# Performance work log

Measured on AMD Instinct MI355X. Metric: run time of the kernel, lower is better.

## Reference

```python
import jax, jax.numpy as jnp
import numpy as np

N = 50000        # n_nodes
E = 1_600_000    # n_edges (before self-loops)
D_IN, HID, HEADS, D_OUT = 32, 64, 4, 32
NEG_SLOPE = 0.2  # PyG GATConv default leaky_relu slope


def setup_inputs() -> dict:
    key = jax.random.key(0)
    ks = jax.random.split(key, 10)
    x = jax.random.normal(ks[0], (N, D_IN), jnp.float32)
    edge_index = jax.random.randint(ks[1], (2, E), 0, N, dtype=jnp.int64)
    s = 0.1
    W_gcn = jax.random.normal(ks[2], (D_IN, HID), jnp.float32) * s
    b_gcn = jnp.zeros((HID,), jnp.float32)
    W_gat = jax.random.normal(ks[3], (HID, HEADS * HID), jnp.float32) * s
    att_src = jax.random.normal(ks[4], (HEADS, HID), jnp.float32) * s
    att_dst = jax.random.normal(ks[5], (HEADS, HID), jnp.float32) * s
    b_gat = jnp.zeros((HEADS * HID,), jnp.float32)
    W_fc = jax.random.normal(ks[6], (HEADS * HID, D_OUT), jnp.float32) * s
    b_fc = jnp.zeros((D_OUT,), jnp.float32)
    return dict(x=x, edge_index=edge_index, W_gcn=W_gcn, b_gcn=b_gcn,
                W_gat=W_gat, att_src=att_src, att_dst=att_dst, b_gat=b_gat,
                W_fc=W_fc, b_fc=b_fc)


def _add_self_loops(edge_index, n):
    loop = jnp.arange(n, dtype=edge_index.dtype)
    src = jnp.concatenate([edge_index[0], loop])
    dst = jnp.concatenate([edge_index[1], loop])
    return src, dst


def _gcn(x, src, dst, W, b):
    h = x @ W                                               # (N, HID)
    deg = jax.ops.segment_sum(jnp.ones_like(src, jnp.float32), dst, N)
    dinv = jnp.where(deg > 0, jax.lax.rsqrt(deg), 0.0)
    norm = dinv[src] * dinv[dst]                            # (E+N,)
    out = jax.ops.segment_sum(h[src] * norm[:, None], dst, N)
    return out + b


def _gat(x, src, dst, W, att_src, att_dst, b):
    h = (x @ W).reshape(N, HEADS, HID)                      # (N, H, C)
    a_s = jnp.einsum('nhc,hc->nh', h, att_src)              # (N, H)
    a_d = jnp.einsum('nhc,hc->nh', h, att_dst)
    e = jax.nn.leaky_relu(a_s[src] + a_d[dst], NEG_SLOPE)   # (E+N, H)
    # softmax over incoming edges per destination node
    m = jax.ops.segment_max(e, dst, N)                      # every dst has a self-loop
    w = jnp.exp(e - m[dst])
    denom = jax.ops.segment_sum(w, dst, N)
    alpha = w / denom[dst]                                  # (E+N, H)
    out = jax.ops.segment_sum(h[src] * alpha[:, :, None], dst, N)
    return out.reshape(N, HEADS * HID) + b


def reference(x, edge_index, W_gcn, b_gcn, W_gat, att_src, att_dst, b_gat, W_fc, b_fc):
    src, dst = _add_self_loops(edge_index, N)
    h = jax.nn.relu(_gcn(x, src, dst, W_gcn, b_gcn))        # dropout: eval mode (identity)
    h = jax.nn.relu(_gat(h, src, dst, W_gat, att_src, att_dst, b_gat))
    return h @ W_fc + b_fc
```

## Files before the change

### kernel.cpp

```cpp
#include <hip/hip_runtime.h>
#include <hip/hip_bf16.h>
#include <hip/hip_fp16.h>
#include <math.h>

#define N_NODES 50000
#define N_EDGES 1600000
#define D_IN    32
#define HID     64
#define HEADS   4
#define D_OUT   32
#define NEG_SLOPE 0.2f
#define CHUNK 128
#define NTILES 3125

#define NBKT 196
#define NBLK_A 391
#define TILE_A 4096
#define GH (NBKT * NBLK_A)
#define NSB 300
#define CAP 10240

typedef _Float16 half8 __attribute__((ext_vector_type(8)));
typedef float    f32x4 __attribute__((ext_vector_type(4)));
typedef float    f32x2 __attribute__((ext_vector_type(2)));

__global__ __launch_bounds__(256) void histA(const int* __restrict__ edge,
                                             int* __restrict__ ghist) {
    __shared__ int hist[4][NBKT];
    int t = threadIdx.x, wv = t >> 6;
    for (int i = t; i < 4 * NBKT; i += 256) ((int*)hist)[i] = 0;
    __syncthreads();
    int base = blockIdx.x * TILE_A;
#pragma unroll
    for (int k = 0; k < 16; k++) {
        int i = base + k * 256 + t;
        if (i < N_EDGES) atomicAdd(&hist[wv][edge[N_EDGES + i] >> 8], 1);
    }
    __syncthreads();
    for (int b = t; b < NBKT; b += 256)
        ghist[b * NBLK_A + blockIdx.x] = hist[0][b] + hist[1][b] + hist[2][b] + hist[3][b];
}

__global__ __launch_bounds__(256) void scanB1(const int* __restrict__ g,
                                              int* __restrict__ bsum) {
    int t = threadIdx.x;
    int i = blockIdx.x * 256 + t;
    int v = (i < GH) ? g[i] : 0;
#pragma unroll
    for (int off = 32; off; off >>= 1) v += __shfl_xor(v, off);
    __shared__ int ws[4];
    if ((t & 63) == 0) ws[t >> 6] = v;
    __syncthreads();
    if (t == 0) bsum[blockIdx.x] = ws[0] + ws[1] + ws[2] + ws[3];
}

__global__ __launch_bounds__(320) void scanB2_attvec(int* __restrict__ bsum,
                                                     const float* __restrict__ W,
                                                     const float* __restrict__ att_s,
                                                     const float* __restrict__ att_d,
                                                     float* __restrict__ vsrc,
                                                     float* __restrict__ vdst) {
    int t = threadIdx.x, lane = t & 63, wv = t >> 6;
    if (blockIdx.x == 0) {
        int v = (t < NSB) ? bsum[t] : 0;
        int inc = v;
#pragma unroll
        for (int d = 1; d < 64; d <<= 1) {
            int u = __shfl_up(inc, d);
            if (lane >= d) inc += u;
        }
        __shared__ int ws[5];
        if (lane == 63) ws[wv] = inc;
        __syncthreads();
        int add = 0;
#pragma unroll
        for (int j = 0; j < 5; j++) if (j < wv) add += ws[j];
        if (t < NSB) bsum[t] = add + inc - v;
    } else if (t < 256) {
        int h = t >> 6, k = t & 63;
        float s_ = 0.f, d_ = 0.f;
#pragma unroll 8
        for (int c = 0; c < 64; c++) {
            float w = W[k * 256 + h * 64 + c];
            s_ += w * att_s[h * 64 + c];
            d_ += w * att_d[h * 64 + c];
        }
        vsrc[h * 64 + k] = s_;
        vdst[h * 64 + k] = d_;
    }
}

__global__ __launch_bounds__(256) void scanB3(int* __restrict__ g,
                                              const int* __restrict__ bsum) {
    int t = threadIdx.x, lane = t & 63, wv = t >> 6;
    int i = blockIdx.x * 256 + t;
    int v = (i < GH) ? g[i] : 0;
    int inc = v;
#pragma unroll
    for (int d = 1; d < 64; d <<= 1) {
        int u = __shfl_up(inc, d);
        if (lane >= d) inc += u;
    }
    __shared__ int ws[4];
    if (lane == 63) ws[wv] = inc;
    __syncthreads();
    int add = 0;
#pragma unroll
    for (int j = 0; j < 4; j++) if (j < wv) add += ws[j];
    if (i < GH) g[i] = bsum[blockIdx.x] + add + inc - v;
}

__global__ __launch_bounds__(256) void scatterC(const int* __restrict__ edge,
                                                const int* __restrict__ ghist,
                                                unsigned* __restrict__ tmp) {
    __shared__ int cur[NBKT];
    int t = threadIdx.x;
    if (t < NBKT) cur[t] = ghist[t * NBLK_A + blockIdx.x];
    __syncthreads();
    int base = blockIdx.x * TILE_A;
#pragma unroll
    for (int k = 0; k < 16; k++) {
        int i = base + k * 256 + t;
        if (i < N_EDGES) {
            int s = edge[i], d = edge[N_EDGES + i];
            int pos = atomicAdd(&cur[d >> 8], 1);
            tmp[pos] = ((unsigned)d << 16) | (unsigned)s;
        }
    }
}

__global__ __launch_bounds__(256) void sortD(const unsigned* __restrict__ tmp,
                                             const int* __restrict__ ghist,
                                             unsigned short* __restrict__ colidx,
                                             int* __restrict__ rowptr,
                                             float* __restrict__ dinv) {
    __shared__ unsigned char  dl8[CAP];
    __shared__ unsigned short s16[CAP];
    __shared__ unsigned short o16[CAP];
    __shared__ int hist[4][256];
    __shared__ int excl[256];
    __shared__ int wsum[4];
    int t = threadIdx.x, lane = t & 63, wv = t >> 6;
    int b = blockIdx.x;
    int lo = ghist[b * NBLK_A];
    int hi = (b < NBKT - 1) ? ghist[(b + 1) * NBLK_A] : N_EDGES;
    int size = hi - lo;
    if (size > CAP) size = CAP;
    for (int i = t; i < 4 * 256; i += 256) ((int*)hist)[i] = 0;
    __syncthreads();
    for (int i = t; i < size; i += 256) {
        unsigned key = tmp[lo + i];
        int dl = (key >> 16) & 255;
        dl8[i] = (unsigned char)dl;
        s16[i] = (unsigned short)(key & 0xFFFF);
        atomicAdd(&hist[wv][dl], 1);
    }
    __syncthreads();
    int h = hist[0][t] + hist[1][t] + hist[2][t] + hist[3][t];
    int inc = h;
#pragma unroll
    for (int d = 1; d < 64; d <<= 1) {
        int u = __shfl_up(inc, d);
        if (lane >= d) inc += u;
    }
    if (lane == 63) wsum[wv] = inc;
    __syncthreads();
    int add = 0;
#pragma unroll
    for (int j = 0; j < 4; j++) if (j < wv) add += wsum[j];
    int ex = inc - h + add;
    excl[t] = ex;
    int node = b * 256 + t;
    if (node < N_NODES) {
        rowptr[node] = lo + ex;
        dinv[node]   = rsqrtf((float)(h + 1));
    }
    if (b == NBKT - 1 && t == 0) rowptr[N_NODES] = N_EDGES;
    __syncthreads();
    for (int i = t; i < size; i += 256) {
        int pos = atomicAdd(&excl[dl8[i]], 1);
        o16[pos] = s16[i];
    }
    __syncthreads();
    for (int i = t; i < size; i += 256) colidx[lo + i] = o16[i];
}

__global__ __launch_bounds__(256) void gemm1(const float* __restrict__ x,
                                             const float* __restrict__ W,
                                             const float* __restrict__ dinv,
                                             __half* __restrict__ h,
                                             __half* __restrict__ h1) {
    __shared__ float Wl[D_IN * HID];
    int t = threadIdx.x;
    if (blockIdx.x == 0 && t < HID) {
        h [(size_t)N_NODES * HID + t] = __float2half(0.f);
        h1[(size_t)N_NODES * HID + t] = __float2half(0.f);
    }
    for (int i = t; i < D_IN * HID; i += 256) Wl[i] = W[i];
    __syncthreads();
    int c = t & 63, rw = t >> 6;
    int r0 = blockIdx.x * 32;
#pragma unroll
    for (int rr = 0; rr < 8; rr++) {
        int r = r0 + rr * 4 + rw;
        if (r >= N_NODES) break;
        const float4* xr4 = (const float4*)(x + r * D_IN);
        float acc = 0.f;
#pragma unroll
        for (int k4 = 0; k4 < D_IN / 4; k4++) {
            float4 xv = xr4[k4];
            int k = k4 * 4;
            acc += xv.x * Wl[(k+0)*HID + c] + xv.y * Wl[(k+1)*HID + c]
                 + xv.z * Wl[(k+2)*HID + c] + xv.w * Wl[(k+3)*HID + c];
        }
        h[r * HID + c] = __float2half(acc * dinv[r]);
    }
}

__global__ __launch_bounds__(256) void gcn_agg(const __half* __restrict__ h,
                                               const int* __restrict__ rowptr,
                                               const unsigned short* __restrict__ colidx,
                                               const float* __restrict__ dinv,
                                               const float* __restrict__ b,
                                               const float* __restrict__ vsrc,
                                               const float* __restrict__ vdst,
                                               __half* __restrict__ h1,
                                               float* __restrict__ as_o,
                                               float* __restrict__ ad_o) {
    __shared__ int sbuf[4][CHUNK + 4];
    int lane = threadIdx.x & 63, wv = threadIdx.x >> 6;
    int quarter = lane >> 4, ql = lane & 15;
    int n = blockIdx.x * 4 + wv;
    if (n >= N_NODES) return;
    int rp = rowptr[n], re = rowptr[n + 1];
    f32x2 a01 = {0.f, 0.f}, a23 = {0.f, 0.f};
    const __half* hp = h + ql * 4;
    for (int cb = rp; cb < re; cb += CHUNK) {
        int ce = min(cb + CHUNK, re);
        for (int e = cb + lane; e < ce; e += 64) sbuf[wv][e - cb] = colidx[e];
        int m = ce - cb;
        int pad = (4 - (m & 3)) & 3;
        if (lane < pad) sbuf[wv][m + lane] = N_NODES;
        int m4 = (m + pad) >> 2;
#pragma unroll 2
        for (int i = 0; i < m4; i++) {
            int s = sbuf[wv][i * 4 + quarter];
            float2 raw = *(const float2*)(hp + s * HID);
            __half2 g0 = __builtin_bit_cast(__half2, raw.x);
            __half2 g1 = __builtin_bit_cast(__half2, raw.y);
            float2 f0 = __half22float2(g0), f1 = __half22float2(g1);
            a01.x += f0.x; a01.y += f0.y;
            a23.x += f1.x; a23.y += f1.y;
        }
    }
#pragma unroll
    for (int off = 16; off <= 32; off <<= 1) {
        a01.x += __shfl_xor(a01.x, off); a01.y += __shfl_xor(a01.y, off);
        a23.x += __shfl_xor(a23.x, off); a23.y += __shfl_xor(a23.y, off);
    }
    if (quarter == 0) {
        float2 raw = *(const float2*)(hp + n * HID);
        __half2 g0 = __builtin_bit_cast(__half2, raw.x);
        __half2 g1 = __builtin_bit_cast(__half2, raw.y);
        float2 f0 = __half22float2(g0), f1 = __half22float2(g1);
        a01.x += f0.x; a01.y += f0.y;
        a23.x += f1.x; a23.y += f1.y;
    }
    float dn = dinv[n];
    const float4 bb = *(const float4*)&b[ql * 4];
    float v0 = fmaxf(a01.x * dn + bb.x, 0.f);
    float v1 = fmaxf(a01.y * dn + bb.y, 0.f);
    float v2 = fmaxf(a23.x * dn + bb.z, 0.f);
    float v3 = fmaxf(a23.y * dn + bb.w, 0.f);
    if (quarter == 0) {
        __half2* op = (__half2*)&h1[n * HID + ql * 4];
        op[0] = __floats2half2_rn(v0, v1);
        op[1] = __floats2half2_rn(v2, v3);
    }
#pragma unroll
    for (int hh = 0; hh < 4; hh++) {
        float4 vsp = *(const float4*)&vsrc[hh * 64 + ql * 4];
        float4 vdp = *(const float4*)&vdst[hh * 64 + ql * 4];
        float vs = v0 * vsp.x + v1 * vsp.y + v2 * vsp.z + v3 * vsp.w;
        float vd = v0 * vdp.x + v1 * vdp.y + v2 * vdp.z + v3 * vdp.w;
#pragma unroll
        for (int off = 8; off > 0; off >>= 1) {
            vs += __shfl_xor(vs, off);
            vd += __shfl_xor(vd, off);
        }
        if (lane == 0) {
            as_o[n * 4 + hh] = vs;
            ad_o[n * 4 + hh] = vd;
        }
    }
}

__global__ __launch_bounds__(256) void gat_agg(const __half* __restrict__ h1,
                                               const int* __restrict__ rowptr,
                                               const unsigned short* __restrict__ colidx,
                                               const float* __restrict__ a_s,
                                               const float* __restrict__ a_d,
                                               __half* __restrict__ u) {
    __shared__ float wbuf[4][(CHUNK + 4) * 4];
    __shared__ int   sbuf[4][CHUNK + 4];
    int lane = threadIdx.x & 63, wv = threadIdx.x >> 6;
    int quarter = lane >> 4, ql = lane & 15;
    int n = blockIdx.x * 4 + wv;
    if (n >= N_NODES) return;
    int rp = rowptr[n], re = rowptr[n + 1];
    float4 ad4 = *(const float4*)&a_d[n * 4];
    float4 asn = *(const float4*)&a_s[n * 4];

    float dnx = 0.f, dny = 0.f, dnz = 0.f, dnw = 0.f;
    f32x2 acc[4][2];
#pragma unroll
    for (int hh = 0; hh < 4; hh++) { acc[hh][0] = (f32x2){0.f,0.f}; acc[hh][1] = (f32x2){0.f,0.f}; }
    const __half* hp = h1 + ql * 4;
    for (int cb = rp; cb < re; cb += CHUNK) {
        int ce = min(cb + CHUNK, re);
        for (int e = cb + lane; e < ce; e += 64) {
            int s = colidx[e];
            float4 a = *(const float4*)&a_s[s * 4];
            float vx = a.x + ad4.x; vx = fmaxf(vx, NEG_SLOPE * vx);
            float vy = a.y + ad4.y; vy = fmaxf(vy, NEG_SLOPE * vy);
            float vz = a.z + ad4.z; vz = fmaxf(vz, NEG_SLOPE * vz);
            float vw = a.w + ad4.w; vw = fmaxf(vw, NEG_SLOPE * vw);
            float wx = __expf(vx), wy = __expf(vy);
            float wz = __expf(vz), ww = __expf(vw);
            dnx += wx; dny += wy; dnz += wz; dnw += ww;
            int idx = e - cb;
            *(float4*)&wbuf[wv][idx * 4] = make_float4(wx, wy, wz, ww);
            sbuf[wv][idx] = s;
        }
        int m = ce - cb;
        int pad = (4 - (m & 3)) & 3;
        if (lane < pad) {
            sbuf[wv][m + lane] = N_NODES;
            *(float4*)&wbuf[wv][(m + lane) * 4] = make_float4(0.f, 0.f, 0.f, 0.f);
        }
        int m4 = (m + pad) >> 2;
#pragma unroll 2
        for (int i = 0; i < m4; i++) {
            int idx = i * 4 + quarter;
            int s = sbuf[wv][idx];
            float4 w4 = *(const float4*)&wbuf[wv][idx * 4];
            float2 raw = *(const float2*)(hp + s * HID);
            __half2 g0 = __builtin_bit_cast(__half2, raw.x);
            __half2 g1 = __builtin_bit_cast(__half2, raw.y);
            float2 t0 = __half22float2(g0), t1 = __half22float2(g1);
            f32x2 f0 = {t0.x, t0.y}, f1 = {t1.x, t1.y};
            f32x2 wx2 = {w4.x, w4.x}, wy2 = {w4.y, w4.y};
            f32x2 wz2 = {w4.z, w4.z}, ww2 = {w4.w, w4.w};
            acc[0][0] += wx2 * f0; acc[0][1] += wx2 * f1;
            acc[1][0] += wy2 * f0; acc[1][1] += wy2 * f1;
            acc[2][0] += wz2 * f0; acc[2][1] += wz2 * f1;
            acc[3][0] += ww2 * f0; acc[3][1] += ww2 * f1;
        }
    }
#pragma unroll
    for (int hh = 0; hh < 4; hh++)
#pragma unroll
        for (int c = 0; c < 2; c++) {
            acc[hh][c].x += __shfl_xor(acc[hh][c].x, 16);
            acc[hh][c].y += __shfl_xor(acc[hh][c].y, 16);
            acc[hh][c].x += __shfl_xor(acc[hh][c].x, 32);
            acc[hh][c].y += __shfl_xor(acc[hh][c].y, 32);
        }
#pragma unroll
    for (int off = 32; off > 0; off >>= 1) {
        dnx += __shfl_xor(dnx, off);
        dny += __shfl_xor(dny, off);
        dnz += __shfl_xor(dnz, off);
        dnw += __shfl_xor(dnw, off);
    }
    float sx = asn.x + ad4.x; sx = fmaxf(sx, NEG_SLOPE * sx);
    float sy = asn.y + ad4.y; sy = fmaxf(sy, NEG_SLOPE * sy);
    float sz = asn.z + ad4.z; sz = fmaxf(sz, NEG_SLOPE * sz);
    float sw = asn.w + ad4.w; sw = fmaxf(sw, NEG_SLOPE * sw);
    float wsx = __expf(sx), wsy = __expf(sy);
    float wsz = __expf(sz), wsw = __expf(sw);
    dnx += wsx; dny += wsy; dnz += wsz; dnw += wsw;
    if (quarter == 0) {
        float2 raw = *(const float2*)(hp + n * HID);
        __half2 g0 = __builtin_bit_cast(__half2, raw.x);
        __half2 g1 = __builtin_bit_cast(__half2, raw.y);
        float2 t0 = __half22float2(g0), t1 = __half22float2(g1);
        acc[0][0].x += wsx * t0.x; acc[0][0].y += wsx * t0.y; acc[0][1].x += wsx * t1.x; acc[0][1].y += wsx * t1.y;
        acc[1][0].x += wsy * t0.x; acc[1][0].y += wsy * t0.y; acc[1][1].x += wsy * t1.x; acc[1][1].y += wsy * t1.y;
        acc[2][0].x += wsz * t0.x; acc[2][0].y += wsz * t0.y; acc[2][1].x += wsz * t1.x; acc[2][1].y += wsz * t1.y;
        acc[3][0].x += wsw * t0.x; acc[3][0].y += wsw * t0.y; acc[3][1].x += wsw * t1.x; acc[3][1].y += wsw * t1.y;
        float r4[4] = {1.f / dnx, 1.f / dny, 1.f / dnz, 1.f / dnw};
        __half* up = u + n * 256 + ql * 4;
#pragma unroll
        for (int hh = 0; hh < 4; hh++) {
            __half2* op = (__half2*)&up[hh * 64];
            op[0] = __floats2half2_rn(acc[hh][0].x * r4[hh], acc[hh][0].y * r4[hh]);
            op[1] = __floats2half2_rn(acc[hh][1].x * r4[hh], acc[hh][1].y * r4[hh]);
        }
    }
}

__global__ __launch_bounds__(256) void gemm2b(const __half* __restrict__ u,
                                              const float* __restrict__ W,
                                              const float* __restrict__ b,
                                              __half* __restrict__ h2) {
    int lane = threadIdx.x & 63, hd = threadIdx.x >> 6;
    int quad = lane >> 4, l16 = lane & 15;
    half8 Bf[4][2];
#pragma unroll
    for (int nt = 0; nt < 4; nt++)
#pragma unroll
        for (int kc = 0; kc < 2; kc++) {
            const float* wp = W + (kc * 32 + quad * 8) * 256 + hd * 64 + nt * 16 + l16;
#pragma unroll
            for (int j = 0; j < 8; j++)
                Bf[nt][kc][j] = (_Float16)wp[j * 256];
        }
    float bb[4];
#pragma unroll
    for (int nt = 0; nt < 4; nt++) bb[nt] = b[hd * 64 + nt * 16 + l16];

    int rt0 = blockIdx.x * 5;
#pragma unroll
    for (int i = 0; i < 5; i++) {
        int rt = rt0 + i;
        const __half* up = u + ((size_t)(rt * 16 + l16)) * 256 + hd * 64 + quad * 8;
        half8 A0 = *(const half8*)(const void*)up;
        half8 A1 = *(const half8*)(const void*)(up + 32);
        f32x4 acc[4];
#pragma unroll
        for (int nt = 0; nt < 4; nt++) {
            acc[nt] = (f32x4){0.f, 0.f, 0.f, 0.f};
            acc[nt] = __builtin_amdgcn_mfma_f32_16x16x32_f16(A0, Bf[nt][0], acc[nt], 0, 0, 0);
            acc[nt] = __builtin_amdgcn_mfma_f32_16x16x32_f16(A1, Bf[nt][1], acc[nt], 0, 0, 0);
        }
#pragma unroll
        for (int nt = 0; nt < 4; nt++) {
            int col = hd * 64 + nt * 16 + l16;
#pragma unroll
            for (int reg = 0; reg < 4; reg++) {
                int row = rt * 16 + quad * 4 + reg;
                h2[(size_t)row * 256 + col] = __float2half(fmaxf(acc[nt][reg] + bb[nt], 0.f));
            }
        }
    }
}

__global__ __launch_bounds__(256) void gemm3(const __half* __restrict__ h2,
                                             const float* __restrict__ W,
                                             const float* __restrict__ b,
                                             float* __restrict__ out) {
    int lane = threadIdx.x & 63, wv = threadIdx.x >> 6;
    int quad = lane >> 4, l16 = lane & 15;
    half8 Bf[2][8];
#pragma unroll
    for (int nt = 0; nt < 2; nt++)
#pragma unroll
        for (int kc = 0; kc < 8; kc++) {
            const float* wp = W + (kc * 32 + quad * 8) * 32 + nt * 16 + l16;
#pragma unroll
            for (int j = 0; j < 8; j++)
                Bf[nt][kc][j] = (_Float16)wp[j * 32];
        }
    float bb0 = b[l16], bb1 = b[16 + l16];

    for (int tile = blockIdx.x * 4 + wv; tile < NTILES; tile += gridDim.x * 4) {
        const __half* hp = h2 + (size_t)(tile * 16 + l16) * 256 + quad * 8;
        f32x4 acc0 = {0.f, 0.f, 0.f, 0.f};
        f32x4 acc1 = {0.f, 0.f, 0.f, 0.f};
#pragma unroll
        for (int kc = 0; kc < 8; kc++) {
            half8 A = *(const half8*)(const void*)(hp + kc * 32);
            acc0 = __builtin_amdgcn_mfma_f32_16x16x32_f16(A, Bf[0][kc], acc0, 0, 0, 0);
            acc1 = __builtin_amdgcn_mfma_f32_16x16x32_f16(A, Bf[1][kc], acc1, 0, 0, 0);
        }
#pragma unroll
        for (int reg = 0; reg < 4; reg++) {
            int row = tile * 16 + quad * 4 + reg;
            out[row * 32 + l16]      = acc0[reg] + bb0;
            out[row * 32 + 16 + l16] = acc1[reg] + bb1;
        }
    }
}

extern "C" void kernel_launch(void* const* d_in, const int* in_sizes, int n_in,
                              void* d_out, int out_size, void* d_ws, size_t ws_size,
                              hipStream_t stream) {
    const float* x      = (const float*)d_in[0];
    const int*   edge   = (const int*)  d_in[1];
    const float* W_gcn  = (const float*)d_in[2];
    const float* b_gcn  = (const float*)d_in[3];
    const float* W_gat  = (const float*)d_in[4];
    const float* att_s  = (const float*)d_in[5];
    const float* att_d  = (const float*)d_in[6];
    const float* b_gat  = (const float*)d_in[7];
    const float* W_fc   = (const float*)d_in[8];
    const float* b_fc   = (const float*)d_in[9];
    float* out = (float*)d_out;

    char* p = (char*)d_ws;
    auto alloc = [&](size_t bytes) {
        char* q = p;
        p += (bytes + 255) & ~(size_t)255;
        return q;
    };
    __half* h     = (__half*)alloc((size_t)(N_NODES + 1) * HID * 2);
    __half* h1    = (__half*)alloc((size_t)(N_NODES + 1) * HID * 2);
    __half* u     = (__half*)alloc((size_t)N_NODES * 256 * 2);
    __half* h2    = (__half*)alloc((size_t)N_NODES * 256 * 2);
    float* as_a   = (float*)alloc((size_t)N_NODES * 4 * 4);
    float* ad_a   = (float*)alloc((size_t)N_NODES * 4 * 4);
    float* dinv   = (float*)alloc((size_t)N_NODES * 4);
    int*   rowptr = (int*)  alloc((size_t)(N_NODES + 1) * 4);
    unsigned short* colidx = (unsigned short*)alloc((size_t)N_EDGES * 2);
    int*   ghist  = (int*)  alloc((size_t)GH * 4);
    int*   bsum   = (int*)  alloc((size_t)NSB * 4);
    unsigned* tmp = (unsigned*)alloc((size_t)N_EDGES * 4);
    float* vsrc   = (float*)alloc((size_t)HEADS * HID * 4);
    float* vdst   = (float*)alloc((size_t)HEADS * HID * 4);

    histA        <<<NBLK_A, 256, 0, stream>>>(edge, ghist);
    scanB1       <<<NSB, 256, 0, stream>>>(ghist, bsum);
    scanB2_attvec<<<2, 320, 0, stream>>>(bsum, W_gat, att_s, att_d, vsrc, vdst);
    scanB3       <<<NSB, 256, 0, stream>>>(ghist, bsum);
    scatterC     <<<NBLK_A, 256, 0, stream>>>(edge, ghist, tmp);
    sortD        <<<NBKT, 256, 0, stream>>>(tmp, ghist, colidx, rowptr, dinv);

    gemm1   <<<(N_NODES + 31) / 32, 256, 0, stream>>>(x, W_gcn, dinv, h, h1);
    gcn_agg <<<(N_NODES + 3) / 4, 256, 0, stream>>>(h, rowptr, colidx, dinv, b_gcn,
                                                    vsrc, vdst, h1, as_a, ad_a);

    gat_agg <<<(N_NODES + 3) / 4, 256, 0, stream>>>(h1, rowptr, colidx, as_a, ad_a, u);
    gemm2b  <<<625, 256, 0, stream>>>(u, W_gat, b_gat, h2);

    gemm3   <<<256, 256, 0, stream>>>(h2, W_fc, b_fc, out);
}
```

Measured before the change: 252.3 us.

## Map one node per quarter-wave in GCN and GAT aggregation kernels

Both aggregation kernels now assign each 16-lane quarter of a wavefront its own destination node (16 nodes per block) instead of one node per wavefront. Each quarter stages its own neighbor indices (premultiplied by HID) and attention weights in shared memory and walks them serially, padding up to the wavefront's maximum degree. This removes the cross-quarter shuffle reductions and the quarter-0-only epilogue, keeping all lanes busy on output. In exchange, degree imbalance among the four nodes in a wavefront causes wasted padded iterations. The bounds check on n was removed, which is safe only because N is divisible by 16.

```diff
diff --git a/kernel.cpp b/kernel.cpp
--- a/kernel.cpp
+++ b/kernel.cpp
@@ -10,8 +10,9 @@
 #define HEADS   4
 #define D_OUT   32
 #define NEG_SLOPE 0.2f
-#define CHUNK 128
 #define NTILES 3125
+
+#define CQ 64
 
 #define NBKT 196
 #define NBLK_A 391
@@ -227,25 +228,29 @@
                                                __half* __restrict__ h1,
                                                float* __restrict__ as_o,
                                                float* __restrict__ ad_o) {
-    __shared__ int sbuf[4][CHUNK + 4];
+    __shared__ int sbuf[4][4][CQ + 1];
     int lane = threadIdx.x & 63, wv = threadIdx.x >> 6;
     int quarter = lane >> 4, ql = lane & 15;
-    int n = blockIdx.x * 4 + wv;
-    if (n >= N_NODES) return;
+    int n = blockIdx.x * 16 + wv * 4 + quarter;
     int rp = rowptr[n], re = rowptr[n + 1];
+    int deg = re - rp;
+    int dm = deg;
+    dm = max(dm, __shfl_xor(dm, 16));
+    dm = max(dm, __shfl_xor(dm, 32));
     f32x2 a01 = {0.f, 0.f}, a23 = {0.f, 0.f};
     const __half* hp = h + ql * 4;
-    for (int cb = rp; cb < re; cb += CHUNK) {
-        int ce = min(cb + CHUNK, re);
-        for (int e = cb + lane; e < ce; e += 64) sbuf[wv][e - cb] = colidx[e];
-        int m = ce - cb;
-        int pad = (4 - (m & 3)) & 3;
-        if (lane < pad) sbuf[wv][m + lane] = N_NODES;
-        int m4 = (m + pad) >> 2;
-#pragma unroll 2
-        for (int i = 0; i < m4; i++) {
-            int s = sbuf[wv][i * 4 + quarter];
-            float2 raw = *(const float2*)(hp + s * HID);
+    int* sq = sbuf[wv][quarter];
+    for (int cb = 0; cb < dm; cb += CQ) {
+        int m  = min(CQ, max(deg - cb, 0));
+        int mm = min(CQ, dm - cb);
+        for (int j = ql; j < m; j += 16)
+            sq[j] = (int)colidx[rp + cb + j] * HID;
+        for (int j = m + ql; j < mm; j += 16)
+            sq[j] = N_NODES * HID;
+#pragma unroll 4
+        for (int i = 0; i < mm; i++) {
+            int off = sq[i];
+            float2 raw = *(const float2*)(hp + off);
             __half2 g0 = __builtin_bit_cast(__half2, raw.x);
             __half2 g1 = __builtin_bit_cast(__half2, raw.y);
             float2 f0 = __half22float2(g0), f1 = __half22float2(g1);
@@ -253,12 +258,7 @@
             a23.x += f1.x; a23.y += f1.y;
         }
     }
-#pragma unroll
-    for (int off = 16; off <= 32; off <<= 1) {
-        a01.x += __shfl_xor(a01.x, off); a01.y += __shfl_xor(a01.y, off);
-        a23.x += __shfl_xor(a23.x, off); a23.y += __shfl_xor(a23.y, off);
-    }
-    if (quarter == 0) {
+    {
         float2 raw = *(const float2*)(hp + n * HID);
         __half2 g0 = __builtin_bit_cast(__half2, raw.x);
         __half2 g1 = __builtin_bit_cast(__half2, raw.y);
@@ -272,11 +272,9 @@
     float v1 = fmaxf(a01.y * dn + bb.y, 0.f);
     float v2 = fmaxf(a23.x * dn + bb.z, 0.f);
     float v3 = fmaxf(a23.y * dn + bb.w, 0.f);
-    if (quarter == 0) {
-        __half2* op = (__half2*)&h1[n * HID + ql * 4];
-        op[0] = __floats2half2_rn(v0, v1);
-        op[1] = __floats2half2_rn(v2, v3);
-    }
+    __half2* op = (__half2*)&h1[n * HID + ql * 4];
+    op[0] = __floats2half2_rn(v0, v1);
+    op[1] = __floats2half2_rn(v2, v3);
 #pragma unroll
     for (int hh = 0; hh < 4; hh++) {
         float4 vsp = *(const float4*)&vsrc[hh * 64 + ql * 4];
@@ -288,7 +286,7 @@
             vs += __shfl_xor(vs, off);
             vd += __shfl_xor(vd, off);
         }
-        if (lane == 0) {
+        if (ql == 0) {
             as_o[n * 4 + hh] = vs;
             ad_o[n * 4 + hh] = vd;
         }
@@ -301,13 +299,16 @@
                                                const float* __restrict__ a_s,
                                                const float* __restrict__ a_d,
                                                __half* __restrict__ u) {
-    __shared__ float wbuf[4][(CHUNK + 4) * 4];
-    __shared__ int   sbuf[4][CHUNK + 4];
+    __shared__ float4 wbuf[4][4][CQ + 1];
+    __shared__ int    sbuf[4][4][CQ + 1];
     int lane = threadIdx.x & 63, wv = threadIdx.x >> 6;
     int quarter = lane >> 4, ql = lane & 15;
-    int n = blockIdx.x * 4 + wv;
-    if (n >= N_NODES) return;
+    int n = blockIdx.x * 16 + wv * 4 + quarter;
     int rp = rowptr[n], re = rowptr[n + 1];
+    int deg = re - rp;
+    int dm = deg;
+    dm = max(dm, __shfl_xor(dm, 16));
+    dm = max(dm, __shfl_xor(dm, 32));
     float4 ad4 = *(const float4*)&a_d[n * 4];
     float4 asn = *(const float4*)&a_s[n * 4];
 
@@ -316,10 +317,13 @@
 #pragma unroll
     for (int hh = 0; hh < 4; hh++) { acc[hh][0] = (f32x2){0.f,0.f}; acc[hh][1] = (f32x2){0.f,0.f}; }
     const __half* hp = h1 + ql * 4;
-    for (int cb = rp; cb < re; cb += CHUNK) {
-        int ce = min(cb + CHUNK, re);
-        for (int e = cb + lane; e < ce; e += 64) {
-            int s = colidx[e];
+    int*    sq = sbuf[wv][quarter];
+    float4* wq = wbuf[wv][quarter];
+    for (int cb = 0; cb < dm; cb += CQ) {
+        int m  = min(CQ, max(deg - cb, 0));
+        int mm = min(CQ, dm - cb);
+        for (int j = ql; j < m; j += 16) {
+            int s = colidx[rp + cb + j];
             float4 a = *(const float4*)&a_s[s * 4];
             float vx = a.x + ad4.x; vx = fmaxf(vx, NEG_SLOPE * vx);
             float vy = a.y + ad4.y; vy = fmaxf(vy, NEG_SLOPE * vy);
@@ -328,23 +332,18 @@
             float wx = __expf(vx), wy = __expf(vy);
             float wz = __expf(vz), ww = __expf(vw);
             dnx += wx; dny += wy; dnz += wz; dnw += ww;
-            int idx = e - cb;
-            *(float4*)&wbuf[wv][idx * 4] = make_float4(wx, wy, wz, ww);
-            sbuf[wv][idx] = s;
-        }
-        int m = ce - cb;
-        int pad = (4 - (m & 3)) & 3;
-        if (lane < pad) {
-            sbuf[wv][m + lane] = N_NODES;
-            *(float4*)&wbuf[wv][(m + lane) * 4] = make_float4(0.f, 0.f, 0.f, 0.f);
-        }
-        int m4 = (m + pad) >> 2;
+            sq[j] = s * HID;
+            wq[j] = make_float4(wx, wy, wz, ww);
+        }
+        for (int j = m + ql; j < mm; j += 16) {
+            sq[j] = N_NODES * HID;
+            wq[j] = make_float4(0.f, 0.f, 0.f, 0.f);
+        }
 #pragma unroll 2
-        for (int i = 0; i < m4; i++) {
-            int idx = i * 4 + quarter;
-            int s = sbuf[wv][idx];
-            float4 w4 = *(const float4*)&wbuf[wv][idx * 4];
-            float2 raw = *(const float2*)(hp + s * HID);
+        for (int i = 0; i < mm; i++) {
+            int off = sq[i];
+            float4 w4 = wq[i];
+            float2 raw = *(const float2*)(hp + off);
             __half2 g0 = __builtin_bit_cast(__half2, raw.x);
             __half2 g1 = __builtin_bit_cast(__half2, raw.y);
             float2 t0 = __half22float2(g0), t1 = __half22float2(g1);
@@ -358,16 +357,7 @@
         }
     }
 #pragma unroll
-    for (int hh = 0; hh < 4; hh++)
-#pragma unroll
-        for (int c = 0; c < 2; c++) {
-            acc[hh][c].x += __shfl_xor(acc[hh][c].x, 16);
-            acc[hh][c].y += __shfl_xor(acc[hh][c].y, 16);
-            acc[hh][c].x += __shfl_xor(acc[hh][c].x, 32);
-            acc[hh][c].y += __shfl_xor(acc[hh][c].y, 32);
-        }
-#pragma unroll
-    for (int off = 32; off > 0; off >>= 1) {
+    for (int off = 8; off > 0; off >>= 1) {
         dnx += __shfl_xor(dnx, off);
         dny += __shfl_xor(dny, off);
         dnz += __shfl_xor(dnz, off);
@@ -380,7 +370,7 @@
     float wsx = __expf(sx), wsy = __expf(sy);
     float wsz = __expf(sz), wsw = __expf(sw);
     dnx += wsx; dny += wsy; dnz += wsz; dnw += wsw;
-    if (quarter == 0) {
+    {
         float2 raw = *(const float2*)(hp + n * HID);
         __half2 g0 = __builtin_bit_cast(__half2, raw.x);
         __half2 g1 = __builtin_bit_cast(__half2, raw.y);
@@ -389,14 +379,14 @@
         acc[1][0].x += wsy * t0.x; acc[1][0].y += wsy * t0.y; acc[1][1].x += wsy * t1.x; acc[1][1].y += wsy * t1.y;
         acc[2][0].x += wsz * t0.x; acc[2][0].y += wsz * t0.y; acc[2][1].x += wsz * t1.x; acc[2][1].y += wsz * t1.y;
         acc[3][0].x += wsw * t0.x; acc[3][0].y += wsw * t0.y; acc[3][1].x += wsw * t1.x; acc[3][1].y += wsw * t1.y;
-        float r4[4] = {1.f / dnx, 1.f / dny, 1.f / dnz, 1.f / dnw};
-        __half* up = u + n * 256 + ql * 4;
-#pragma unroll
-        for (int hh = 0; hh < 4; hh++) {
-            __half2* op = (__half2*)&up[hh * 64];
-            op[0] = __floats2half2_rn(acc[hh][0].x * r4[hh], acc[hh][0].y * r4[hh]);
-            op[1] = __floats2half2_rn(acc[hh][1].x * r4[hh], acc[hh][1].y * r4[hh]);
-        }
+    }
+    float r4[4] = {1.f / dnx, 1.f / dny, 1.f / dnz, 1.f / dnw};
+    __half* up = u + n * 256 + ql * 4;
+#pragma unroll
+    for (int hh = 0; hh < 4; hh++) {
+        __half2* op = (__half2*)&up[hh * 64];
+        op[0] = __floats2half2_rn(acc[hh][0].x * r4[hh], acc[hh][0].y * r4[hh]);
+        op[1] = __floats2half2_rn(acc[hh][1].x * r4[hh], acc[hh][1].y * r4[hh]);
     }
 }
 
@@ -527,10 +517,10 @@
     sortD        <<<NBKT, 256, 0, stream>>>(tmp, ghist, colidx, rowptr, dinv);
 
     gemm1   <<<(N_NODES + 31) / 32, 256, 0, stream>>>(x, W_gcn, dinv, h, h1);
-    gcn_agg <<<(N_NODES + 3) / 4, 256, 0, stream>>>(h, rowptr, colidx, dinv, b_gcn,
-                                                    vsrc, vdst, h1, as_a, ad_a);
-
-    gat_agg <<<(N_NODES + 3) / 4, 256, 0, stream>>>(h1, rowptr, colidx, as_a, ad_a, u);
+    gcn_agg <<<(N_NODES + 15) / 16, 256, 0, stream>>>(h, rowptr, colidx, dinv, b_gcn,
+                                                      vsrc, vdst, h1, as_a, ad_a);
+
+    gat_agg <<<(N_NODES + 15) / 16, 256, 0, stream>>>(h1, rowptr, colidx, as_a, ad_a, u);
     gemm2b  <<<625, 256, 0, stream>>>(u, W_gat, b_gat, h2);
 
     gemm3   <<<256, 256, 0, stream>>>(h2, W_fc, b_fc, out);
```

Result: faster. 227.1 us (-10.0%).
